# Kernel optimization log

Measured on AMD Instinct MI355X. Metric: run time of the kernel, lower is better.

The kernel has to match this reference:

```python
import jax, jax.numpy as jnp
import numpy as np

H = 4  # num_heads
EPS = 1e-12


def _mhsa(x, wq, bq, wk, bk, wv, bv, wo, bo):
    # x: [N, A, B, E]; attention over axis B within each (N, A)
    N, A, B, E = x.shape
    d = E // H
    q = (x @ wq + bq).reshape(N, A, B, H, d)
    k = (x @ wk + bk).reshape(N, A, B, H, d)
    v = (x @ wv + bv).reshape(N, A, B, H, d)
    s = jnp.einsum('naqhd,nakhd->nahqk', q, k) / (d ** 0.5)
    a = jax.nn.softmax(s, axis=-1)
    o = jnp.einsum('nahqk,nakhd->naqhd', a, v).reshape(N, A, B, E)
    return o @ wo + bo


def setup_inputs() -> dict:
    key = jax.random.key(0)
    ks = jax.random.split(key, 32)
    N, C, T, V, E, NC = 1024, 3, 30, 14, 64, 7
    g = lambda k, shape, s=0.05: (jax.random.normal(k, shape, dtype=jnp.float32) * s)
    inp = {
        'x_joint': jax.random.normal(ks[0], (N, C, T, V), dtype=jnp.float32),
        'x_vel': jax.random.normal(ks[1], (N, C, T, V), dtype=jnp.float32),
        'je_w': g(ks[2], (C, E)), 'je_b': g(ks[3], (E,)),
        've_w': g(ks[4], (C, E)), 've_b': g(ks[5], (E,)),
        'joint_emb': g(ks[6], (V, E)), 'frame_emb': g(ks[7], (T, E)),
        'proj_w': g(ks[8], (3 * E, E)), 'proj_b': g(ks[9], (E,)),
        'gcn_w1': g(ks[10], (E, E)), 'gcn_b1': g(ks[11], (E,)),
        'gcn_w2': g(ks[12], (E, E)), 'gcn_b2': g(ks[13], (E,)),
        'sa_wq': g(ks[14], (E, E)), 'sa_bq': g(ks[15], (E,)),
        'sa_wk': g(ks[16], (E, E)), 'sa_bk': g(ks[17], (E,)),
        'sa_wv': g(ks[18], (E, E)), 'sa_bv': g(ks[19], (E,)),
        'sa_wo': g(ks[20], (E, E)), 'sa_bo': g(ks[21], (E,)),
        'ta_wq': g(ks[22], (E, E)), 'ta_bq': g(ks[23], (E,)),
        'ta_wk': g(ks[24], (E, E)), 'ta_bk': g(ks[25], (E,)),
        'ta_wv': g(ks[26], (E, E)), 'ta_bv': g(ks[27], (E,)),
        'ta_wo': g(ks[28], (E, E)), 'ta_bo': g(ks[29], (E,)),
        'fc_w': g(ks[30], (E, NC)), 'fc_b': g(ks[31], (NC,)),
    }
    return inp


def reference(x_joint, x_vel, je_w, je_b, ve_w, ve_b, joint_emb, frame_emb,
              proj_w, proj_b, gcn_w1, gcn_b1, gcn_w2, gcn_b2,
              sa_wq, sa_bq, sa_wk, sa_bk, sa_wv, sa_bv, sa_wo, sa_bo,
              ta_wq, ta_bq, ta_wk, ta_bk, ta_wv, ta_bv, ta_wo, ta_bo,
              fc_w, fc_b):
    N, C, T, V = x_joint.shape
    E = je_w.shape[1]
    # 1x1 convs (pointwise over channels) -> [N, T, V, E]
    f = (jnp.einsum('nctv,ce->ntve', x_joint, je_w) + je_b
         + jnp.einsum('nctv,ce->ntve', x_vel, ve_w) + ve_b)
    jE = jnp.broadcast_to(joint_emb[None, None, :, :], (N, T, V, E))
    fE = jnp.broadcast_to(frame_emb[None, :, None, :], (N, T, V, E))
    feat = jnp.concatenate([f, jE, fE], axis=-1) @ proj_w + proj_b  # [N,T,V,E]
    # attention adjacency over joints per frame
    nf = feat / jnp.maximum(jnp.linalg.norm(feat, axis=-1, keepdims=True), EPS)
    adj = jax.nn.softmax(nf @ jnp.swapaxes(nf, -1, -2), axis=-1)  # [N,T,V,V]
    feat = adj @ feat
    feat = jax.nn.relu(feat @ gcn_w1 + gcn_b1) @ gcn_w2 + gcn_b2
    # spatial attention (over V) with residual
    feat = _mhsa(feat, sa_wq, sa_bq, sa_wk, sa_bk, sa_wv, sa_bv, sa_wo, sa_bo) + feat
    # temporal attention (over T) with residual
    ft = jnp.swapaxes(feat, 1, 2)  # [N,V,T,E]
    ft = _mhsa(ft, ta_wq, ta_bq, ta_wk, ta_bk, ta_wv, ta_bv, ta_wo, ta_bo) + ft
    feat = jnp.swapaxes(ft, 1, 2)  # [N,T,V,E]
    pooled = jnp.max(feat, axis=(1, 2))  # adaptive max pool over (T,V)
    return pooled @ fc_w + fc_b
```

## Files before the change

### kernel.cpp

```cpp
#include <hip/hip_runtime.h>
#include <math.h>

#define C_ 3
#define T_ 30
#define V_ 14
#define E_ 64
#define H_ 4
#define D_ 16
#define NC_ 7

#define SW_ 72
#define SV_ 20

typedef unsigned short u16;
typedef __attribute__((ext_vector_type(8))) short bf16x8;
typedef __attribute__((ext_vector_type(4))) short bf16x4;
typedef __attribute__((ext_vector_type(4))) float f32x4;
typedef __attribute__((ext_vector_type(16))) float f32x16;

__device__ __forceinline__ float4 f4_load(const float* p) {
    return *reinterpret_cast<const float4*>(p);
}
__device__ __forceinline__ float4 f4_add(float4 a, float4 b) {
    return make_float4(a.x + b.x, a.y + b.y, a.z + b.z, a.w + b.w);
}
__device__ __forceinline__ float4 f4_fma(float a, float4 b, float4 c) {
    c.x = fmaf(a, b.x, c.x); c.y = fmaf(a, b.y, c.y);
    c.z = fmaf(a, b.z, c.z); c.w = fmaf(a, b.w, c.w); return c;
}
__device__ __forceinline__ u16 f2bf(float x) {
    union { __bf16 b; u16 u; } cv;
    cv.b = (__bf16)x;
    return cv.u;
}
__device__ __forceinline__ uint2 pack4bf(float4 f) {
    return make_uint2((unsigned)f2bf(f.x) | ((unsigned)f2bf(f.y) << 16),
                      (unsigned)f2bf(f.z) | ((unsigned)f2bf(f.w) << 16));
}
__device__ __forceinline__ f32x16 f16z() {
    return (f32x16){0.f,0.f,0.f,0.f, 0.f,0.f,0.f,0.f, 0.f,0.f,0.f,0.f, 0.f,0.f,0.f,0.f};
}
__device__ __forceinline__ bf16x8 ld_frag8(const u16* p) {
    bf16x4 lo = *(const bf16x4*)p;
    bf16x4 hi = *(const bf16x4*)(p + 4);
    return __builtin_shufflevector(lo, hi, 0, 1, 2, 3, 4, 5, 6, 7);
}

__global__ void k_setup(const float* __restrict__ je_w, const float* __restrict__ je_b,
                        const float* __restrict__ ve_w, const float* __restrict__ ve_b,
                        const float* __restrict__ joint_emb, const float* __restrict__ frame_emb,
                        const float* __restrict__ proj_w, const float* __restrict__ proj_b,
                        const float* __restrict__ twq, const float* __restrict__ twk,
                        const float* __restrict__ twv, const float* __restrict__ two,
                        const float* __restrict__ sw1, const float* __restrict__ sw2,
                        const float* __restrict__ swq, const float* __restrict__ swk,
                        const float* __restrict__ swv, const float* __restrict__ swo,
                        float* __restrict__ tab) {
    int e = threadIdx.x;
    int b = blockIdx.x;
    if (b >= 1 && b <= 10) {
        int m = b - 1;
        const float* Ws[10] = {twq, twk, twv, two, sw1, sw2, swq, swk, swv, swo};
        const float* W = Ws[m];
        u16* wt = (u16*)(tab + 3200);
        for (int i = 0; i < E_; ++i)
            wt[m * 4096 + e * 64 + i] = f2bf(W[i * E_ + e]);
        return;
    }
    if (b >= 11) {
        float bias = proj_b[e];
        for (int i = 0; i < E_; ++i) bias += (je_b[i] + ve_b[i]) * proj_w[i * E_ + e];
        int t0 = (b - 11) * 10;
        for (int t = t0; t < t0 + 10; ++t) {
            float s = bias;
            for (int i = 0; i < E_; ++i) s += frame_emb[t * E_ + i] * proj_w[(128 + i) * E_ + e];
            tab[1280 + t * E_ + e] = s;
        }
        return;
    }
    for (int c = 0; c < C_; ++c) {
        float aj = 0.f, av = 0.f;
        for (int i = 0; i < E_; ++i) {
            float p0 = proj_w[i * E_ + e];
            aj += je_w[c * E_ + i] * p0;
            av += ve_w[c * E_ + i] * p0;
        }
        tab[c * E_ + e] = aj;
        tab[192 + c * E_ + e] = av;
    }
    for (int v = 0; v < V_; ++v) {
        float s = 0.f;
        for (int i = 0; i < E_; ++i) s += joint_emb[v * E_ + i] * proj_w[(64 + i) * E_ + e];
        tab[384 + v * E_ + e] = s;
    }
}

__global__ __launch_bounds__(128) void k_spatial(
    const float* __restrict__ xj, const float* __restrict__ xv,
    const float* __restrict__ tab, const u16* __restrict__ wt16,
    const float* __restrict__ b1, const float* __restrict__ b2,
    const float* __restrict__ bq, const float* __restrict__ bk,
    const float* __restrict__ bv, const float* __restrict__ bo,
    float* __restrict__ feat1) {
    int ntb = blockIdx.x;
    int n = ntb / T_;
    int t = ntb % T_;
    int tid = threadIdx.x;
    int wid = tid >> 6;
    int lane = tid & 63;
    int dcol = lane & 15;
    int kgrp = (lane >> 4) & 3;
    int trow4 = kgrp * 4;
    int e4 = dcol << 2;
    int r4 = kgrp;
    int l32 = lane & 31;
    int half = (lane >> 5) & 1;

    const u16* w1T = wt16 + 4 * 4096;
    const u16* w2T = wt16 + 5 * 4096;
    const u16* wqT = wt16 + 6 * 4096;
    const u16* wkT = wt16 + 7 * 4096;
    const u16* wvT = wt16 + 8 * 4096;
    const u16* woT = wt16 + 9 * 4096;

    __shared__ __align__(16) u16 sm[6272];
    u16* feat16 = sm;
    u16* g1out  = sm;
    u16* ao16   = sm;
    u16* fT16   = sm + 1152;
    u16* qkvin  = sm + 1152;
    float* adjraw = (float*)(sm + 2432);
    u16* g1in   = sm + 2432;
    u16* qs16   = sm + 2432;
    u16* ps16   = sm + 2432;
    float* scb  = (float*)sm;
    u16* adjs16 = sm + 3712;
    u16* ks16   = sm + 3712;
    u16* vsT16  = sm + 4992;
    float* xs   = (float*)(sm + 4992);

    for (int o = tid; o < 2 * C_ * V_; o += 128) {
        int s = o / (C_ * V_);
        int rem = o % (C_ * V_);
        int c = rem / V_, v = rem % V_;
        const float* src = s ? xv : xj;
        xs[(s * C_ + c) * V_ + v] = src[((size_t)(n * C_ + c) * T_ + t) * V_ + v];
    }
    __syncthreads();

    {
        float4 F = f4_load(tab + 1280 + t * E_ + e4);
        float4 AJ[C_], AV[C_];
#pragma unroll
        for (int c = 0; c < C_; ++c) {
            AJ[c] = f4_load(tab + c * E_ + e4);
            AV[c] = f4_load(tab + 192 + c * E_ + e4);
        }
#pragma unroll
        for (int j = 0; j < 2; ++j) {
            int q = r4 + 4 * (wid * 2 + j);
            if (q < V_) {
                float4 s = f4_add(F, f4_load(tab + 384 + q * E_ + e4));
#pragma unroll
                for (int c = 0; c < C_; ++c) {
                    s = f4_fma(xs[(0 * C_ + c) * V_ + q], AJ[c], s);
                    s = f4_fma(xs[(1 * C_ + c) * V_ + q], AV[c], s);
                }
                *(uint2*)&feat16[q * SW_ + e4] = pack4bf(s);
                fT16[(e4 + 0) * SV_ + q] = f2bf(s.x);
                fT16[(e4 + 1) * SV_ + q] = f2bf(s.y);
                fT16[(e4 + 2) * SV_ + q] = f2bf(s.z);
                fT16[(e4 + 3) * SV_ + q] = f2bf(s.w);
            }
        }
        if (wid == 0) {
            fT16[lane * SV_ + 14] = 0;
            fT16[lane * SV_ + 15] = 0;
        }
    }
    __syncthreads();

    if (wid == 0) {
        bf16x8 f0 = *(bf16x8*)&feat16[dcol * SW_ + kgrp * 8];
        bf16x8 f1 = *(bf16x8*)&feat16[dcol * SW_ + 32 + kgrp * 8];
        f32x4 d = (f32x4){0.f, 0.f, 0.f, 0.f};
        d = __builtin_amdgcn_mfma_f32_16x16x32_bf16(f0, f0, d, 0, 0, 0);
        d = __builtin_amdgcn_mfma_f32_16x16x32_bf16(f1, f1, d, 0, 0, 0);
#pragma unroll
        for (int r = 0; r < 4; ++r) {
            int row = trow4 + r;
            if (row < V_) adjraw[row * 18 + dcol] = d[r];
        }
    }
    __syncthreads();

    if (tid < 4 * V_) {
        int row = tid >> 2, g = tid & 3;
        float iq = 1.0f / fmaxf(sqrtf(adjraw[row * 18 + row]), 1e-12f);
        float c[4];
        float m = -1e30f;
#pragma unroll
        for (int j = 0; j < 4; ++j) {
            int k = g * 4 + j;
            if (k < V_) {
                float ik = 1.0f / fmaxf(sqrtf(adjraw[k * 18 + k]), 1e-12f);
                c[j] = adjraw[row * 18 + k] * iq * ik;
            } else {
                c[j] = -1e30f;
            }
            m = fmaxf(m, c[j]);
        }
        m = fmaxf(m, __shfl_xor(m, 1));
        m = fmaxf(m, __shfl_xor(m, 2));
        float su = 0.f;
#pragma unroll
        for (int j = 0; j < 4; ++j) { c[j] = __expf(c[j] - m); su += c[j]; }
        su += __shfl_xor(su, 1);
        su += __shfl_xor(su, 2);
        float iv = 1.f / su;
#pragma unroll
        for (int j = 0; j < 4; ++j) {
            int k = g * 4 + j;
            if (k < V_) adjs16[row * SV_ + k] = f2bf(c[j] * iv);
        }
        if (g == 3) {
            adjs16[row * SV_ + 14] = 0;
            adjs16[row * SV_ + 15] = 0;
        }
    }
    __syncthreads();

    {
        bf16x8 aA = ld_frag8(&adjs16[l32 * SV_ + half * 8]);
        int nt = wid;
        bf16x8 bB = ld_frag8(&fT16[(nt * 32 + l32) * SV_ + half * 8]);
        f32x16 g = f16z();
        g = __builtin_amdgcn_mfma_f32_32x32x16_bf16(aA, bB, g, 0, 0, 0);
#pragma unroll
        for (int reg = 0; reg < 16; ++reg) {
            int row = (reg & 3) + 8 * (reg >> 2) + 4 * half;
            if (row < V_) g1in[row * SW_ + nt * 32 + l32] = f2bf(g[reg]);
        }
    }
    __syncthreads();

    {
        bf16x8 a0 = *(bf16x8*)&g1in[dcol * SW_ + kgrp * 8];
        bf16x8 a1 = *(bf16x8*)&g1in[dcol * SW_ + 32 + kgrp * 8];
#pragma unroll
        for (int j = 0; j < 2; ++j) {
            int nt = wid * 2 + j;
            int col = nt * 16 + dcol;
            float bb = b1[col];
            f32x4 cc = (f32x4){bb, bb, bb, bb};
            cc = __builtin_amdgcn_mfma_f32_16x16x32_bf16(a0, *(const bf16x8*)&w1T[col * 64 + kgrp * 8], cc, 0, 0, 0);
            cc = __builtin_amdgcn_mfma_f32_16x16x32_bf16(a1, *(const bf16x8*)&w1T[col * 64 + 32 + kgrp * 8], cc, 0, 0, 0);
#pragma unroll
            for (int r = 0; r < 4; ++r) {
                int row = trow4 + r;
                if (row < V_) g1out[row * SW_ + col] = f2bf(fmaxf(cc[r], 0.f));
            }
        }
    }
    __syncthreads();

    f32x4 fresr[2];
    {
        bf16x8 a0 = *(bf16x8*)&g1out[dcol * SW_ + kgrp * 8];
        bf16x8 a1 = *(bf16x8*)&g1out[dcol * SW_ + 32 + kgrp * 8];
#pragma unroll
        for (int j = 0; j < 2; ++j) {
            int nt = wid * 2 + j;
            int col = nt * 16 + dcol;
            float bb = b2[col];
            f32x4 cc = (f32x4){bb, bb, bb, bb};
            cc = __builtin_amdgcn_mfma_f32_16x16x32_bf16(a0, *(const bf16x8*)&w2T[col * 64 + kgrp * 8], cc, 0, 0, 0);
            cc = __builtin_amdgcn_mfma_f32_16x16x32_bf16(a1, *(const bf16x8*)&w2T[col * 64 + 32 + kgrp * 8], cc, 0, 0, 0);
            fresr[j] = cc;
#pragma unroll
            for (int r = 0; r < 4; ++r) {
                int row = trow4 + r;
                if (row < V_) qkvin[row * SW_ + col] = f2bf(cc[r]);
            }
        }
    }
    __syncthreads();

    {
        bf16x8 a0 = *(bf16x8*)&qkvin[dcol * SW_ + kgrp * 8];
        bf16x8 a1 = *(bf16x8*)&qkvin[dcol * SW_ + 32 + kgrp * 8];
#pragma unroll
        for (int j = 0; j < 2; ++j) {
            int nt = wid * 2 + j;
            int col = nt * 16 + dcol;
            float bqs = bq[col], bks = bk[col], bvs = bv[col];
            f32x4 cq = (f32x4){bqs, bqs, bqs, bqs};
            f32x4 ck = (f32x4){bks, bks, bks, bks};
            f32x4 cv = (f32x4){bvs, bvs, bvs, bvs};
            cq = __builtin_amdgcn_mfma_f32_16x16x32_bf16(a0, *(const bf16x8*)&wqT[col * 64 + kgrp * 8], cq, 0, 0, 0);
            cq = __builtin_amdgcn_mfma_f32_16x16x32_bf16(a1, *(const bf16x8*)&wqT[col * 64 + 32 + kgrp * 8], cq, 0, 0, 0);
            ck = __builtin_amdgcn_mfma_f32_16x16x32_bf16(a0, *(const bf16x8*)&wkT[col * 64 + kgrp * 8], ck, 0, 0, 0);
            ck = __builtin_amdgcn_mfma_f32_16x16x32_bf16(a1, *(const bf16x8*)&wkT[col * 64 + 32 + kgrp * 8], ck, 0, 0, 0);
            cv = __builtin_amdgcn_mfma_f32_16x16x32_bf16(a0, *(const bf16x8*)&wvT[col * 64 + kgrp * 8], cv, 0, 0, 0);
            cv = __builtin_amdgcn_mfma_f32_16x16x32_bf16(a1, *(const bf16x8*)&wvT[col * 64 + 32 + kgrp * 8], cv, 0, 0, 0);
            int pair = wid, hw = j;
            u16* qsb = qs16 + pair * 640;
            u16* ksb = ks16 + pair * 640;
            u16* vtb = vsT16 + pair * 640;
#pragma unroll
            for (int r = 0; r < 4; ++r) {
                int row = trow4 + r;
                qsb[(hw * 16 + row) * SV_ + dcol] = f2bf(cq[r]);
                ksb[(hw * 16 + row) * SV_ + dcol] = f2bf(ck[r]);
                vtb[(hw * 16 + dcol) * SV_ + row] = (row < V_) ? f2bf(cv[r]) : (u16)0;
            }
        }
    }
    __syncthreads();

    {
        int pair = wid;
        bf16x8 aq = ld_frag8(&qs16[pair * 640 + l32 * SV_ + half * 8]);
        bf16x8 bk8 = ld_frag8(&ks16[pair * 640 + l32 * SV_ + half * 8]);
        f32x16 d = f16z();
        d = __builtin_amdgcn_mfma_f32_32x32x16_bf16(aq, bk8, d, 0, 0, 0);
        int kp = l32 & 15, hp = l32 >> 4;
        if (kp < V_) {
#pragma unroll
            for (int reg = 0; reg < 16; ++reg) {
                int row = (reg & 3) + 8 * (reg >> 2) + 4 * half;
                if ((row >> 4) == hp && (row & 15) < V_)
                    scb[(pair * 2 + hp) * 252 + (row & 15) * 18 + kp] = d[reg];
            }
        }
    }
    __syncthreads();

    if (lane < 2 * V_) {
        int h = wid * 2 + lane / V_, q = lane % V_;
        float p[V_];
        float m = -1e30f;
#pragma unroll
        for (int k = 0; k < V_; ++k) { p[k] = scb[h * 252 + q * 18 + k]; m = fmaxf(m, p[k]); }
        float su = 0.f;
#pragma unroll
        for (int k = 0; k < V_; ++k) { p[k] = __expf((p[k] - m) * 0.25f); su += p[k]; }
        float iv = 1.f / su;
        u16* psb = ps16 + wid * 640;
        int rowp = (h & 1) * 16 + q;
#pragma unroll
        for (int k = 0; k < V_; ++k) psb[rowp * SV_ + k] = f2bf(p[k] * iv);
        psb[rowp * SV_ + 14] = 0;
        psb[rowp * SV_ + 15] = 0;
    }
    __syncthreads();

    {
        int pair = wid;
        bf16x8 ap = ld_frag8(&ps16[pair * 640 + l32 * SV_ + half * 8]);
        bf16x8 bv8 = ld_frag8(&vsT16[pair * 640 + l32 * SV_ + half * 8]);
        f32x16 d = f16z();
        d = __builtin_amdgcn_mfma_f32_32x32x16_bf16(ap, bv8, d, 0, 0, 0);
        int np = l32 & 15, hp = l32 >> 4;
#pragma unroll
        for (int reg = 0; reg < 16; ++reg) {
            int row = (reg & 3) + 8 * (reg >> 2) + 4 * half;
            if ((row >> 4) == hp && (row & 15) < V_)
                ao16[(row & 15) * SW_ + (pair * 2 + hp) * 16 + np] = f2bf(d[reg]);
        }
    }
    __syncthreads();

    {
        bf16x8 a0 = *(bf16x8*)&ao16[dcol * SW_ + kgrp * 8];
        bf16x8 a1 = *(bf16x8*)&ao16[dcol * SW_ + 32 + kgrp * 8];
        float* dst = feat1 + (size_t)ntb * (V_ * E_);
#pragma unroll
        for (int j = 0; j < 2; ++j) {
            int nt = wid * 2 + j;
            int col = nt * 16 + dcol;
            float bos = bo[col];
            f32x4 cc = (f32x4){bos, bos, bos, bos};
            cc = __builtin_amdgcn_mfma_f32_16x16x32_bf16(a0, *(const bf16x8*)&woT[col * 64 + kgrp * 8], cc, 0, 0, 0);
            cc = __builtin_amdgcn_mfma_f32_16x16x32_bf16(a1, *(const bf16x8*)&woT[col * 64 + 32 + kgrp * 8], cc, 0, 0, 0);
#pragma unroll
            for (int r = 0; r < 4; ++r) {
                int row = trow4 + r;
                if (row < V_) dst[row * E_ + col] = cc[r] + fresr[j][r];
            }
        }
    }
}

__global__ __launch_bounds__(64) void k_temporal(
    const float* __restrict__ feat1,
    const u16* __restrict__ wt16,
    const float* __restrict__ bq, const float* __restrict__ bk,
    const float* __restrict__ bv, const float* __restrict__ bo,
    float* __restrict__ tmax) {
    int nv = blockIdx.x;
    int n = nv / V_;
    int v = nv % V_;
    int tid = threadIdx.x;
    int dcol = tid & 15;
    int kgrp = tid >> 4;
    int trow4 = kgrp * 4;
    int l32 = tid & 31;
    int half = tid >> 5;

    const u16* wtq = wt16;
    const u16* wtk = wt16 + 4096;
    const u16* wtv = wt16 + 8192;
    const u16* wto = wt16 + 12288;

    __shared__ __align__(16) u16 smt[6464];
    u16*  ft16 = smt;
    float* scb = (float*)smt;
    u16*  ao16 = smt + 2304;
    u16*  qs16 = smt + 4608;
    u16*  ks16 = smt + 5248;
    u16*  ps16 = smt + 4608;
    u16*  vT16 = smt + 5888;

    const float* fsrc = feat1 + ((size_t)n * T_ * V_ + v) * E_;

    for (int o = tid; o < T_ * 16; o += 64) {
        int t = o >> 4, c4i = (o & 15) << 2;
        float4 f = f4_load(fsrc + (size_t)t * V_ * E_ + c4i);
        *(uint2*)&ft16[t * 72 + c4i] = pack4bf(f);
    }
    __syncthreads();

    bf16x8 af[2][2];
#pragma unroll
    for (int mt = 0; mt < 2; ++mt)
#pragma unroll
        for (int ks = 0; ks < 2; ++ks)
            af[mt][ks] = *(bf16x8*)&ft16[(mt * 16 + dcol) * 72 + ks * 32 + kgrp * 8];

    bool sact = (tid < 2 * T_);
    int sq = sact ? (tid >> 1) : 0;
    int kbase = (tid & 1) * 15;

    for (int h = 0; h < H_; ++h) {
        {
            float bqs = bq[h * D_ + dcol];
            float bks = bk[h * D_ + dcol];
            f32x4 qacc[2], kacc[2];
#pragma unroll
            for (int mt = 0; mt < 2; ++mt) {
                qacc[mt] = (f32x4){bqs, bqs, bqs, bqs};
                kacc[mt] = (f32x4){bks, bks, bks, bks};
            }
#pragma unroll
            for (int ks = 0; ks < 2; ++ks) {
                int boff = (h * D_ + dcol) * 64 + ks * 32 + kgrp * 8;
                bf16x8 b_q = *(const bf16x8*)&wtq[boff];
                bf16x8 b_k = *(const bf16x8*)&wtk[boff];
#pragma unroll
                for (int mt = 0; mt < 2; ++mt) {
                    qacc[mt] = __builtin_amdgcn_mfma_f32_16x16x32_bf16(af[mt][ks], b_q, qacc[mt], 0, 0, 0);
                    kacc[mt] = __builtin_amdgcn_mfma_f32_16x16x32_bf16(af[mt][ks], b_k, kacc[mt], 0, 0, 0);
                }
            }
#pragma unroll
            for (int mt = 0; mt < 2; ++mt)
#pragma unroll
                for (int r = 0; r < 4; ++r) {
                    int t = mt * 16 + trow4 + r;
                    qs16[t * SV_ + dcol] = f2bf(qacc[mt][r]);
                    ks16[t * SV_ + dcol] = f2bf(kacc[mt][r]);
                }
        }
        __syncthreads();

        {
            bf16x8 aq = ld_frag8(&qs16[l32 * SV_ + half * 8]);
            bf16x8 bk8 = ld_frag8(&ks16[l32 * SV_ + half * 8]);
            f32x16 d = f16z();
            d = __builtin_amdgcn_mfma_f32_32x32x16_bf16(aq, bk8, d, 0, 0, 0);
            if (l32 < T_) {
#pragma unroll
                for (int reg = 0; reg < 16; ++reg) {
                    int row = (reg & 3) + 8 * (reg >> 2) + 4 * half;
                    if (row < T_) scb[row * 36 + l32] = d[reg];
                }
            }
        }
        __syncthreads();

        {
            float m = -1e30f;
#pragma unroll
            for (int k = 0; k < 15; ++k) m = fmaxf(m, scb[sq * 36 + kbase + k]);
            m = fmaxf(m, __shfl_xor(m, 1));
            float ex[15];
            float su = 0.f;
#pragma unroll
            for (int k = 0; k < 15; ++k) {
                ex[k] = __expf((scb[sq * 36 + kbase + k] - m) * 0.25f);
                su += ex[k];
            }
            su += __shfl_xor(su, 1);
            float iv = 1.f / su;
            if (sact) {
#pragma unroll
                for (int k = 0; k < 15; ++k) ps16[sq * 36 + kbase + k] = f2bf(ex[k] * iv);
                if (kbase) { ps16[sq * 36 + 30] = 0; ps16[sq * 36 + 31] = 0; }
            }
        }
        {
            float bvs = bv[h * D_ + dcol];
            f32x4 vacc[2];
            vacc[0] = (f32x4){bvs, bvs, bvs, bvs};
            vacc[1] = vacc[0];
#pragma unroll
            for (int ks = 0; ks < 2; ++ks) {
                int boff = (h * D_ + dcol) * 64 + ks * 32 + kgrp * 8;
                bf16x8 b_v = *(const bf16x8*)&wtv[boff];
#pragma unroll
                for (int mt = 0; mt < 2; ++mt)
                    vacc[mt] = __builtin_amdgcn_mfma_f32_16x16x32_bf16(af[mt][ks], b_v, vacc[mt], 0, 0, 0);
            }
#pragma unroll
            for (int mt = 0; mt < 2; ++mt)
#pragma unroll
                for (int r = 0; r < 4; ++r) {
                    int t = mt * 16 + trow4 + r;
                    vT16[dcol * 36 + t] = (t < T_) ? f2bf(vacc[mt][r]) : (u16)0;
                }
        }
        __syncthreads();

        {
            bf16x8 ap0 = ld_frag8(&ps16[l32 * 36 + half * 8]);
            bf16x8 ap1 = ld_frag8(&ps16[l32 * 36 + 16 + half * 8]);
            bf16x8 bv0 = ld_frag8(&vT16[(l32 & 15) * 36 + half * 8]);
            bf16x8 bv1 = ld_frag8(&vT16[(l32 & 15) * 36 + 16 + half * 8]);
            f32x16 d = f16z();
            d = __builtin_amdgcn_mfma_f32_32x32x16_bf16(ap0, bv0, d, 0, 0, 0);
            d = __builtin_amdgcn_mfma_f32_32x32x16_bf16(ap1, bv1, d, 0, 0, 0);
            if (l32 < 16) {
#pragma unroll
                for (int reg = 0; reg < 16; ++reg) {
                    int row = (reg & 3) + 8 * (reg >> 2) + 4 * half;
                    if (row < T_) ao16[row * 72 + h * D_ + l32] = f2bf(d[reg]);
                }
            }
        }
        __syncthreads();
    }

    {
        bf16x8 oa[2][2];
#pragma unroll
        for (int mt = 0; mt < 2; ++mt)
#pragma unroll
            for (int ks = 0; ks < 2; ++ks)
                oa[mt][ks] = *(bf16x8*)&ao16[(mt * 16 + dcol) * 72 + ks * 32 + kgrp * 8];

        float mxc[4];
#pragma unroll
        for (int nt = 0; nt < 4; ++nt) {
            float bos = bo[nt * 16 + dcol];
            f32x4 oacc[2];
            oacc[0] = (f32x4){bos, bos, bos, bos};
            oacc[1] = oacc[0];
#pragma unroll
            for (int ks = 0; ks < 2; ++ks) {
                bf16x8 bb = *(const bf16x8*)&wto[(nt * 16 + dcol) * 64 + ks * 32 + kgrp * 8];
#pragma unroll
                for (int mt = 0; mt < 2; ++mt)
                    oacc[mt] = __builtin_amdgcn_mfma_f32_16x16x32_bf16(oa[mt][ks], bb, oacc[mt], 0, 0, 0);
            }
            float m = -1e30f;
#pragma unroll
            for (int mt = 0; mt < 2; ++mt)
#pragma unroll
                for (int r = 0; r < 4; ++r) {
                    int t = mt * 16 + trow4 + r;
                    if (t < T_) {
                        float rr = oacc[mt][r] +
                                   fsrc[(size_t)t * V_ * E_ + nt * 16 + dcol];
                        m = fmaxf(m, rr);
                    }
                }
            mxc[nt] = m;
        }
#pragma unroll
        for (int nt = 0; nt < 4; ++nt) {
            mxc[nt] = fmaxf(mxc[nt], __shfl_xor(mxc[nt], 16));
            mxc[nt] = fmaxf(mxc[nt], __shfl_xor(mxc[nt], 32));
        }
        if (tid < 16) {
#pragma unroll
            for (int nt = 0; nt < 4; ++nt)
                tmax[(size_t)nv * E_ + nt * 16 + tid] = mxc[nt];
        }
    }
}

__global__ void k_pool_fc(const float* __restrict__ tmax,
                          const float* __restrict__ fc_w, const float* __restrict__ fc_b,
                          float* __restrict__ out) {
    int n = blockIdx.x;
    int tid = threadIdx.x;
    __shared__ float pooled[E_];
    float m = -1e30f;
    for (int v = 0; v < V_; ++v) m = fmaxf(m, tmax[((size_t)n * V_ + v) * E_ + tid]);
    pooled[tid] = m;
    __syncthreads();
    if (tid < NC_) {
        float s = fc_b[tid];
        for (int e = 0; e < E_; ++e) s += pooled[e] * fc_w[e * NC_ + tid];
        out[n * NC_ + tid] = s;
    }
}

extern "C" void kernel_launch(void* const* d_in, const int* in_sizes, int n_in,
                              void* d_out, int out_size, void* d_ws, size_t ws_size,
                              hipStream_t stream) {
    const float* xj        = (const float*)d_in[0];
    const float* xv        = (const float*)d_in[1];
    const float* je_w      = (const float*)d_in[2];
    const float* je_b      = (const float*)d_in[3];
    const float* ve_w      = (const float*)d_in[4];
    const float* ve_b      = (const float*)d_in[5];
    const float* joint_emb = (const float*)d_in[6];
    const float* frame_emb = (const float*)d_in[7];
    const float* proj_w    = (const float*)d_in[8];
    const float* proj_b    = (const float*)d_in[9];
    const float* gcn_w1    = (const float*)d_in[10];
    const float* gcn_b1    = (const float*)d_in[11];
    const float* gcn_w2    = (const float*)d_in[12];
    const float* gcn_b2    = (const float*)d_in[13];
    const float* sa_wq     = (const float*)d_in[14];
    const float* sa_bq     = (const float*)d_in[15];
    const float* sa_wk     = (const float*)d_in[16];
    const float* sa_bk     = (const float*)d_in[17];
    const float* sa_wv     = (const float*)d_in[18];
    const float* sa_bv     = (const float*)d_in[19];
    const float* sa_wo     = (const float*)d_in[20];
    const float* sa_bo     = (const float*)d_in[21];
    const float* ta_wq     = (const float*)d_in[22];
    const float* ta_bq     = (const float*)d_in[23];
    const float* ta_wk     = (const float*)d_in[24];
    const float* ta_bk     = (const float*)d_in[25];
    const float* ta_wv     = (const float*)d_in[26];
    const float* ta_bv     = (const float*)d_in[27];
    const float* ta_wo     = (const float*)d_in[28];
    const float* ta_bo     = (const float*)d_in[29];
    const float* fc_w      = (const float*)d_in[30];
    const float* fc_b      = (const float*)d_in[31];
    float* out = (float*)d_out;

    int N = in_sizes[0] / (C_ * T_ * V_);

    float* ws    = (float*)d_ws;
    float* tab   = ws;
    u16*   wt16  = (u16*)(ws + 3200);
    float* tmax  = ws + 3200 + 20480;
    float* feat1 = tmax + (size_t)N * V_ * E_;

    k_setup<<<14, 64, 0, stream>>>(je_w, je_b, ve_w, ve_b, joint_emb, frame_emb,
                                   proj_w, proj_b,
                                   ta_wq, ta_wk, ta_wv, ta_wo,
                                   gcn_w1, gcn_w2, sa_wq, sa_wk, sa_wv, sa_wo, tab);
    k_spatial<<<N * T_, 128, 0, stream>>>(xj, xv, tab, wt16,
                                          gcn_b1, gcn_b2,
                                          sa_bq, sa_bk, sa_bv, sa_bo, feat1);
    k_temporal<<<N * V_, 64, 0, stream>>>(feat1, wt16,
                                          ta_bq, ta_bk, ta_bv, ta_bo, tmax);
    k_pool_fc<<<N, 64, 0, stream>>>(tmax, fc_w, fc_b, out);
}
```

Measured before the change: 353.1 us.

## Process two (n,t) frames per spatial block to amortize syncs and weight loads

The spatial kernel now handles two consecutive (n,t) frames per 128-thread block, each with its own shared-memory arena, and launches half as many blocks. Stages that previously ran on only one wave (Gram matrix, adjacency softmax) now give one frame to each wave, and the other stages loop over both frames. This amortizes barriers, launch overhead and global weight-fragment loads over twice the work. In exchange shared memory doubles, register pressure rises from the per-frame residual arrays, and there is half as much block-level parallelism.

```diff
diff --git a/kernel.cpp b/kernel.cpp
--- a/kernel.cpp
+++ b/kernel.cpp
@@ -11,6 +11,7 @@
 
 #define SW_ 72
 #define SV_ 20
+#define ARN_ 6272
 
 typedef unsigned short u16;
 typedef __attribute__((ext_vector_type(8))) short bf16x8;
@@ -102,9 +103,7 @@
     const float* __restrict__ bq, const float* __restrict__ bk,
     const float* __restrict__ bv, const float* __restrict__ bo,
     float* __restrict__ feat1) {
-    int ntb = blockIdx.x;
-    int n = ntb / T_;
-    int t = ntb % T_;
+    int ntb0 = blockIdx.x * 2;
     int tid = threadIdx.x;
     int wid = tid >> 6;
     int lane = tid & 63;
@@ -123,33 +122,27 @@
     const u16* wvT = wt16 + 8 * 4096;
     const u16* woT = wt16 + 9 * 4096;
 
-    __shared__ __align__(16) u16 sm[6272];
-    u16* feat16 = sm;
-    u16* g1out  = sm;
-    u16* ao16   = sm;
-    u16* fT16   = sm + 1152;
-    u16* qkvin  = sm + 1152;
-    float* adjraw = (float*)(sm + 2432);
-    u16* g1in   = sm + 2432;
-    u16* qs16   = sm + 2432;
-    u16* ps16   = sm + 2432;
-    float* scb  = (float*)sm;
-    u16* adjs16 = sm + 3712;
-    u16* ks16   = sm + 3712;
-    u16* vsT16  = sm + 4992;
-    float* xs   = (float*)(sm + 4992);
-
-    for (int o = tid; o < 2 * C_ * V_; o += 128) {
-        int s = o / (C_ * V_);
-        int rem = o % (C_ * V_);
-        int c = rem / V_, v = rem % V_;
+    __shared__ __align__(16) u16 sm[2 * ARN_];
+
+    int tt[2];
+    tt[0] = ntb0 % T_;
+    tt[1] = (ntb0 + 1) % T_;
+    int nn0 = ntb0 / T_, nn1 = (ntb0 + 1) / T_;
+
+    for (int o = tid; o < 2 * 2 * C_ * V_; o += 128) {
+        int tl = o / (2 * C_ * V_);
+        int rem = o % (2 * C_ * V_);
+        int s = rem / (C_ * V_);
+        int r2 = rem % (C_ * V_);
+        int c = r2 / V_, v = r2 % V_;
         const float* src = s ? xv : xj;
-        xs[(s * C_ + c) * V_ + v] = src[((size_t)(n * C_ + c) * T_ + t) * V_ + v];
+        int n = tl ? nn1 : nn0;
+        float* xs = (float*)(sm + tl * ARN_ + 4992);
+        xs[(s * C_ + c) * V_ + v] = src[((size_t)(n * C_ + c) * T_ + tt[tl]) * V_ + v];
     }
     __syncthreads();
 
     {
-        float4 F = f4_load(tab + 1280 + t * E_ + e4);
         float4 AJ[C_], AV[C_];
 #pragma unroll
         for (int c = 0; c < C_; ++c) {
@@ -157,30 +150,42 @@
             AV[c] = f4_load(tab + 192 + c * E_ + e4);
         }
 #pragma unroll
-        for (int j = 0; j < 2; ++j) {
-            int q = r4 + 4 * (wid * 2 + j);
-            if (q < V_) {
-                float4 s = f4_add(F, f4_load(tab + 384 + q * E_ + e4));
-#pragma unroll
-                for (int c = 0; c < C_; ++c) {
-                    s = f4_fma(xs[(0 * C_ + c) * V_ + q], AJ[c], s);
-                    s = f4_fma(xs[(1 * C_ + c) * V_ + q], AV[c], s);
+        for (int tl = 0; tl < 2; ++tl) {
+            u16* A = sm + tl * ARN_;
+            u16* feat16 = A;
+            u16* fT16 = A + 1152;
+            float* xs = (float*)(A + 4992);
+            float4 F = f4_load(tab + 1280 + tt[tl] * E_ + e4);
+#pragma unroll
+            for (int j = 0; j < 2; ++j) {
+                int q = r4 + 4 * (wid * 2 + j);
+                if (q < V_) {
+                    float4 s = f4_add(F, f4_load(tab + 384 + q * E_ + e4));
+#pragma unroll
+                    for (int c = 0; c < C_; ++c) {
+                        s = f4_fma(xs[(0 * C_ + c) * V_ + q], AJ[c], s);
+                        s = f4_fma(xs[(1 * C_ + c) * V_ + q], AV[c], s);
+                    }
+                    *(uint2*)&feat16[q * SW_ + e4] = pack4bf(s);
+                    fT16[(e4 + 0) * SV_ + q] = f2bf(s.x);
+                    fT16[(e4 + 1) * SV_ + q] = f2bf(s.y);
+                    fT16[(e4 + 2) * SV_ + q] = f2bf(s.z);
+                    fT16[(e4 + 3) * SV_ + q] = f2bf(s.w);
                 }
-                *(uint2*)&feat16[q * SW_ + e4] = pack4bf(s);
-                fT16[(e4 + 0) * SV_ + q] = f2bf(s.x);
-                fT16[(e4 + 1) * SV_ + q] = f2bf(s.y);
-                fT16[(e4 + 2) * SV_ + q] = f2bf(s.z);
-                fT16[(e4 + 3) * SV_ + q] = f2bf(s.w);
-            }
-        }
-        if (wid == 0) {
+            }
+        }
+        {
+            u16* fT16 = sm + wid * ARN_ + 1152;
             fT16[lane * SV_ + 14] = 0;
             fT16[lane * SV_ + 15] = 0;
         }
     }
     __syncthreads();
 
-    if (wid == 0) {
+    {
+        u16* A = sm + wid * ARN_;
+        u16* feat16 = A;
+        float* adjraw = (float*)(A + 2432);
         bf16x8 f0 = *(bf16x8*)&feat16[dcol * SW_ + kgrp * 8];
         bf16x8 f1 = *(bf16x8*)&feat16[dcol * SW_ + 32 + kgrp * 8];
         f32x4 d = (f32x4){0.f, 0.f, 0.f, 0.f};
@@ -194,8 +199,11 @@
     }
     __syncthreads();
 
-    if (tid < 4 * V_) {
-        int row = tid >> 2, g = tid & 3;
+    if (lane < 4 * V_) {
+        u16* A = sm + wid * ARN_;
+        float* adjraw = (float*)(A + 2432);
+        u16* adjs16 = A + 3712;
+        int row = lane >> 2, g = lane & 3;
         float iq = 1.0f / fmaxf(sqrtf(adjraw[row * 18 + row]), 1e-12f);
         float c[4];
         float m = -1e30f;
@@ -230,7 +238,12 @@
     }
     __syncthreads();
 
-    {
+#pragma unroll
+    for (int tl = 0; tl < 2; ++tl) {
+        u16* A = sm + tl * ARN_;
+        u16* adjs16 = A + 3712;
+        u16* fT16 = A + 1152;
+        u16* g1in = A + 2432;
         bf16x8 aA = ld_frag8(&adjs16[l32 * SV_ + half * 8]);
         int nt = wid;
         bf16x8 bB = ld_frag8(&fT16[(nt * 32 + l32) * SV_ + half * 8]);
@@ -244,7 +257,11 @@
     }
     __syncthreads();
 
-    {
+#pragma unroll
+    for (int tl = 0; tl < 2; ++tl) {
+        u16* A = sm + tl * ARN_;
+        u16* g1in = A + 2432;
+        u16* g1out = A;
         bf16x8 a0 = *(bf16x8*)&g1in[dcol * SW_ + kgrp * 8];
         bf16x8 a1 = *(bf16x8*)&g1in[dcol * SW_ + 32 + kgrp * 8];
 #pragma unroll
@@ -264,8 +281,12 @@
     }
     __syncthreads();
 
-    f32x4 fresr[2];
-    {
+    f32x4 fresr[2][2];
+#pragma unroll
+    for (int tl = 0; tl < 2; ++tl) {
+        u16* A = sm + tl * ARN_;
+        u16* g1out = A;
+        u16* qkvin = A + 1152;
         bf16x8 a0 = *(bf16x8*)&g1out[dcol * SW_ + kgrp * 8];
         bf16x8 a1 = *(bf16x8*)&g1out[dcol * SW_ + 32 + kgrp * 8];
 #pragma unroll
@@ -276,7 +297,7 @@
             f32x4 cc = (f32x4){bb, bb, bb, bb};
             cc = __builtin_amdgcn_mfma_f32_16x16x32_bf16(a0, *(const bf16x8*)&w2T[col * 64 + kgrp * 8], cc, 0, 0, 0);
             cc = __builtin_amdgcn_mfma_f32_16x16x32_bf16(a1, *(const bf16x8*)&w2T[col * 64 + 32 + kgrp * 8], cc, 0, 0, 0);
-            fresr[j] = cc;
+            fresr[tl][j] = cc;
 #pragma unroll
             for (int r = 0; r < 4; ++r) {
                 int row = trow4 + r;
@@ -286,7 +307,13 @@
     }
     __syncthreads();
 
-    {
+#pragma unroll
+    for (int tl = 0; tl < 2; ++tl) {
+        u16* A = sm + tl * ARN_;
+        u16* qkvin = A + 1152;
+        u16* qs16 = A + 2432;
+        u16* ks16 = A + 3712;
+        u16* vsT16 = A + 4992;
         bf16x8 a0 = *(bf16x8*)&qkvin[dcol * SW_ + kgrp * 8];
         bf16x8 a1 = *(bf16x8*)&qkvin[dcol * SW_ + 32 + kgrp * 8];
 #pragma unroll
@@ -318,7 +345,12 @@
     }
     __syncthreads();
 
-    {
+#pragma unroll
+    for (int tl = 0; tl < 2; ++tl) {
+        u16* A = sm + tl * ARN_;
+        u16* qs16 = A + 2432;
+        u16* ks16 = A + 3712;
+        float* scb = (float*)A;
         int pair = wid;
         bf16x8 aq = ld_frag8(&qs16[pair * 640 + l32 * SV_ + half * 8]);
         bf16x8 bk8 = ld_frag8(&ks16[pair * 640 + l32 * SV_ + half * 8]);
@@ -336,26 +368,37 @@
     }
     __syncthreads();
 
-    if (lane < 2 * V_) {
-        int h = wid * 2 + lane / V_, q = lane % V_;
-        float p[V_];
-        float m = -1e30f;
-#pragma unroll
-        for (int k = 0; k < V_; ++k) { p[k] = scb[h * 252 + q * 18 + k]; m = fmaxf(m, p[k]); }
-        float su = 0.f;
-#pragma unroll
-        for (int k = 0; k < V_; ++k) { p[k] = __expf((p[k] - m) * 0.25f); su += p[k]; }
-        float iv = 1.f / su;
-        u16* psb = ps16 + wid * 640;
-        int rowp = (h & 1) * 16 + q;
-#pragma unroll
-        for (int k = 0; k < V_; ++k) psb[rowp * SV_ + k] = f2bf(p[k] * iv);
-        psb[rowp * SV_ + 14] = 0;
-        psb[rowp * SV_ + 15] = 0;
-    }
-    __syncthreads();
-
-    {
+#pragma unroll
+    for (int tl = 0; tl < 2; ++tl) {
+        if (lane < 2 * V_) {
+            u16* A = sm + tl * ARN_;
+            float* scb = (float*)A;
+            u16* ps16 = A + 2432;
+            int h = wid * 2 + lane / V_, q = lane % V_;
+            float p[V_];
+            float m = -1e30f;
+#pragma unroll
+            for (int k = 0; k < V_; ++k) { p[k] = scb[h * 252 + q * 18 + k]; m = fmaxf(m, p[k]); }
+            float su = 0.f;
+#pragma unroll
+            for (int k = 0; k < V_; ++k) { p[k] = __expf((p[k] - m) * 0.25f); su += p[k]; }
+            float iv = 1.f / su;
+            u16* psb = ps16 + wid * 640;
+            int rowp = (h & 1) * 16 + q;
+#pragma unroll
+            for (int k = 0; k < V_; ++k) psb[rowp * SV_ + k] = f2bf(p[k] * iv);
+            psb[rowp * SV_ + 14] = 0;
+            psb[rowp * SV_ + 15] = 0;
+        }
+    }
+    __syncthreads();
+
+#pragma unroll
+    for (int tl = 0; tl < 2; ++tl) {
+        u16* A = sm + tl * ARN_;
+        u16* ps16 = A + 2432;
+        u16* vsT16 = A + 4992;
+        u16* ao16 = A;
         int pair = wid;
         bf16x8 ap = ld_frag8(&ps16[pair * 640 + l32 * SV_ + half * 8]);
         bf16x8 bv8 = ld_frag8(&vsT16[pair * 640 + l32 * SV_ + half * 8]);
@@ -371,10 +414,13 @@
     }
     __syncthreads();
 
-    {
+#pragma unroll
+    for (int tl = 0; tl < 2; ++tl) {
+        u16* A = sm + tl * ARN_;
+        u16* ao16 = A;
         bf16x8 a0 = *(bf16x8*)&ao16[dcol * SW_ + kgrp * 8];
         bf16x8 a1 = *(bf16x8*)&ao16[dcol * SW_ + 32 + kgrp * 8];
-        float* dst = feat1 + (size_t)ntb * (V_ * E_);
+        float* dst = feat1 + (size_t)(ntb0 + tl) * (V_ * E_);
 #pragma unroll
         for (int j = 0; j < 2; ++j) {
             int nt = wid * 2 + j;
@@ -386,7 +432,7 @@
 #pragma unroll
             for (int r = 0; r < 4; ++r) {
                 int row = trow4 + r;
-                if (row < V_) dst[row * E_ + col] = cc[r] + fresr[j][r];
+                if (row < V_) dst[row * E_ + col] = cc[r] + fresr[tl][j][r];
             }
         }
     }
@@ -666,9 +712,9 @@
                                    proj_w, proj_b,
                                    ta_wq, ta_wk, ta_wv, ta_wo,
                                    gcn_w1, gcn_w2, sa_wq, sa_wk, sa_wv, sa_wo, tab);
-    k_spatial<<<N * T_, 128, 0, stream>>>(xj, xv, tab, wt16,
-                                          gcn_b1, gcn_b2,
-                                          sa_bq, sa_bk, sa_bv, sa_bo, feat1);
+    k_spatial<<<N * T_ / 2, 128, 0, stream>>>(xj, xv, tab, wt16,
+                                              gcn_b1, gcn_b2,
+                                              sa_bq, sa_bk, sa_bv, sa_bo, feat1);
     k_temporal<<<N * V_, 64, 0, stream>>>(feat1, wt16,
                                           ta_bq, ta_bk, ta_bv, ta_bo, tmax);
     k_pool_fc<<<N, 64, 0, stream>>>(tmax, fc_w, fc_b, out);
```

After: 325.0 us, median of 2. 8.0% less time.
